# Kernel tuning notes

Hardware: AMD Instinct MI355X
Metric: run time of the kernel (lower is better)

## Reference

```python
import jax, jax.numpy as jnp
import numpy as np

N = 4096
INPLANES = 256
PLANES = 256
LOC_PLANES = 256


def _ln(x, g, b, eps=1e-5):
    m = jnp.mean(x, axis=-1, keepdims=True)
    v = jnp.mean(jnp.square(x - m), axis=-1, keepdims=True)
    return (x - m) * jax.lax.rsqrt(v + eps) * g + b


def setup_inputs() -> dict:
    key = jax.random.key(0)
    ks = jax.random.split(key, 12)
    s = 0.02
    cat_dim = INPLANES + LOC_PLANES
    return {
        "img_fea": jax.random.normal(ks[0], (N, INPLANES), jnp.float32),
        "loc_fea": jax.random.normal(ks[1], (N, LOC_PLANES), jnp.float32),
        # conv11: Basic1d(cat_dim -> inplanes, bias=True) + ReLU
        "w11": jax.random.normal(ks[2], (cat_dim, INPLANES), jnp.float32) * s,
        "b11": jnp.zeros((INPLANES,), jnp.float32),
        # conv12: Linear(inplanes -> inplanes)
        "w12": jax.random.normal(ks[3], (INPLANES, INPLANES), jnp.float32) * s,
        "b12": jnp.zeros((INPLANES,), jnp.float32),
        # conv21: Basic1d(cat_dim -> inplanes, bias=True) + ReLU
        "w21": jax.random.normal(ks[4], (cat_dim, INPLANES), jnp.float32) * s,
        "b21": jnp.zeros((INPLANES,), jnp.float32),
        # conv22: Linear(inplanes -> inplanes*planes) -- hypernetwork weight generator
        "w22": jax.random.normal(ks[5], (INPLANES, INPLANES * PLANES), jnp.float32) * s,
        "b22": jnp.zeros((INPLANES * PLANES,), jnp.float32),
        # br: LayerNorm(planes)
        "lnbr_g": jnp.ones((PLANES,), jnp.float32),
        "lnbr_b": jnp.zeros((PLANES,), jnp.float32),
        # conv3: Basic1d(planes -> planes, bias=False) -> Linear + LayerNorm + ReLU
        "w3": jax.random.normal(ks[6], (PLANES, PLANES), jnp.float32) * s,
        "ln3_g": jnp.ones((PLANES,), jnp.float32),
        "ln3_b": jnp.zeros((PLANES,), jnp.float32),
    }


def reference(img_fea, loc_fea, w11, b11, w12, b12, w21, b21, w22, b22,
              lnbr_g, lnbr_b, w3, ln3_g, ln3_b):
    cat = jnp.concatenate([img_fea, loc_fea], axis=1)          # [N, 512]
    h11 = jax.nn.relu(cat @ w11 + b11)                          # [N, 256]
    wgt12 = h11 @ w12 + b12                                     # [N, 256]
    h21 = jax.nn.relu(cat @ w21 + b21)                          # [N, 256]
    wgt22 = (h21 @ w22 + b22).reshape(-1, INPLANES, PLANES)     # [N, 256, 256]
    out = jnp.einsum('bi,bio->bo', wgt12, wgt22)                # batched GEMV
    out = jax.nn.relu(_ln(out, lnbr_g, lnbr_b))
    out = jax.nn.relu(_ln(out @ w3, ln3_g, ln3_b))
    return (out, loc_fea)
```

## Files before the change

kernel.cpp:

```cpp
#include <hip/hip_runtime.h>
#include <stdint.h>

typedef unsigned short u16;
typedef __bf16 bf16;
typedef bf16 bf16x8 __attribute__((ext_vector_type(8)));
typedef u16 u16x8 __attribute__((ext_vector_type(8)));
typedef float f32x4 __attribute__((ext_vector_type(4)));

__device__ __forceinline__ u16 f2bf(float f) {
  union { float f; unsigned u; } v; v.f = f;
  unsigned u = v.u;
  u += 0x7FFFu + ((u >> 16) & 1u);
  return (u16)(u >> 16);
}

__device__ __forceinline__ bf16x8 as_bf16x8(u16x8 v) {
  return __builtin_bit_cast(bf16x8, v);
}

__device__ __forceinline__ f32x4 mfma16(bf16x8 a, bf16x8 b, f32x4 c) {
  return __builtin_amdgcn_mfma_f32_16x16x32_bf16(a, b, c, 0, 0, 0);
}

__global__ __launch_bounds__(256) void k_transpose(const float* __restrict__ src,
    u16* __restrict__ dst, long dstStride, long dstOff) {
  __shared__ float tile[64][65];
  const int t = threadIdx.x;
  const int tr = t >> 6, tc = t & 63;
  const long rb = (long)blockIdx.x * 64;
  const int ob = blockIdx.y * 64;
#pragma unroll
  for (int i = 0; i < 16; ++i) {
    int r = i * 4 + tr;
    tile[r][tc] = src[(rb + r) * 256 + ob + tc];
  }
  __syncthreads();
  const int orow = t >> 2, seg = t & 3;
#pragma unroll
  for (int h = 0; h < 2; ++h) {
    u16x8 v;
#pragma unroll
    for (int j = 0; j < 8; ++j) v[j] = f2bf(tile[seg * 16 + h * 8 + j][orow]);
    *(u16x8*)&dst[(long)(ob + orow) * dstStride + dstOff + rb + seg * 16 + h * 8] = v;
  }
}

__global__ __launch_bounds__(256) void k_transpose_multi(
    const float* __restrict__ b22, const float* __restrict__ w11,
    const float* __restrict__ w21, const float* __restrict__ w12,
    const float* __restrict__ w3, u16* __restrict__ W2T, u16* __restrict__ W11T,
    u16* __restrict__ W21T, u16* __restrict__ W12T, u16* __restrict__ W3T) {
  __shared__ float tile[64][65];
  const int x = blockIdx.x;
  const float* src; u16* dst; long stride, off; int rb;
  if (x < 4)       { src = b22; dst = W2T;  stride = 65792; off = 65536; rb = x; }
  else if (x < 12) { src = w11; dst = W11T; stride = 512;   off = 0;     rb = x - 4; }
  else if (x < 20) { src = w21; dst = W21T; stride = 512;   off = 0;     rb = x - 12; }
  else if (x < 24) { src = w12; dst = W12T; stride = 256;   off = 0;     rb = x - 20; }
  else             { src = w3;  dst = W3T;  stride = 256;   off = 0;     rb = x - 24; }
  const long rbase = (long)rb * 64;
  const int t = threadIdx.x;
  const int tr = t >> 6, tc = t & 63;
  const int ob = blockIdx.y * 64;
#pragma unroll
  for (int i = 0; i < 16; ++i) {
    int r = i * 4 + tr;
    tile[r][tc] = src[(rbase + r) * 256 + ob + tc];
  }
  __syncthreads();
  const int orow = t >> 2, seg = t & 3;
#pragma unroll
  for (int h = 0; h < 2; ++h) {
    u16x8 v;
#pragma unroll
    for (int j = 0; j < 8; ++j) v[j] = f2bf(tile[seg * 16 + h * 8 + j][orow]);
    *(u16x8*)&dst[(long)(ob + orow) * stride + off + rbase + seg * 16 + h * 8] = v;
  }
}

__device__ __forceinline__ void gemm_small_core(const float* A0, const float* A1,
    int K, const u16* WT, f32x4 (&acc)[4], int o0, long row) {
  const int lane = threadIdx.x & 63;
  const int l15 = lane & 15, lhi = lane >> 4;
  const int kg = lhi * 8;
  for (int ks = 0; ks < K; ks += 32) {
    int k = ks + kg;
    const float* ap = (A1 != nullptr && k >= 256) ? (A1 + row * 256 + (k - 256))
                                                  : (A0 + row * 256 + k);
    f32x4 f0 = *(const f32x4*)ap;
    f32x4 f1 = *(const f32x4*)(ap + 4);
    u16x8 a;
    a[0]=f2bf(f0[0]); a[1]=f2bf(f0[1]); a[2]=f2bf(f0[2]); a[3]=f2bf(f0[3]);
    a[4]=f2bf(f1[0]); a[5]=f2bf(f1[1]); a[6]=f2bf(f1[2]); a[7]=f2bf(f1[3]);
    bf16x8 av = as_bf16x8(a);
#pragma unroll
    for (int nf = 0; nf < 4; ++nf) {
      int o = o0 + nf * 16 + l15;
      u16x8 braw = *(const u16x8*)(WT + (long)o * K + k);
      acc[nf] = mfma16(av, as_bf16x8(braw), acc[nf]);
    }
  }
}

__global__ __launch_bounds__(256) void k_gemm_pair(const float* __restrict__ img,
    const float* __restrict__ loc, const u16* __restrict__ W11T,
    const float* __restrict__ b11, float* __restrict__ h11,
    const u16* __restrict__ W21T, const float* __restrict__ b21,
    float* __restrict__ h21) {
  const int t = threadIdx.x;
  const int wid = t >> 6, lane = t & 63;
  const int l15 = lane & 15, lhi = lane >> 4;
  const int b0 = blockIdx.x * 16;
  const int o0 = wid * 64;
  const long row = b0 + l15;
  const u16* WT = (blockIdx.y == 0) ? W11T : W21T;
  const float* bias = (blockIdx.y == 0) ? b11 : b21;
  float* out = (blockIdx.y == 0) ? h11 : h21;
  f32x4 acc[4] = {};
  gemm_small_core(img, loc, 512, WT, acc, o0, row);
#pragma unroll
  for (int nf = 0; nf < 4; ++nf) {
    int o = o0 + nf * 16 + l15;
    float bs = bias[o];
#pragma unroll
    for (int r = 0; r < 4; ++r) {
      long b = b0 + lhi * 4 + r;
      out[b * 256 + o] = fmaxf(acc[nf][r] + bs, 0.f);
    }
  }
}

__global__ __launch_bounds__(256) void k_gemm_wgt12(const float* __restrict__ h11,
    const u16* __restrict__ W12T, const float* __restrict__ b12,
    u16* __restrict__ wgt12B) {
  const int t = threadIdx.x;
  const int wid = t >> 6, lane = t & 63;
  const int l15 = lane & 15, lhi = lane >> 4;
  const int b0 = blockIdx.x * 16;
  const int o0 = wid * 64;
  const long row = b0 + l15;
  f32x4 acc[4] = {};
  gemm_small_core(h11, nullptr, 256, W12T, acc, o0, row);
#pragma unroll
  for (int nf = 0; nf < 4; ++nf) {
    int o = o0 + nf * 16 + l15;
    float bs = b12[o];
#pragma unroll
    for (int r = 0; r < 4; ++r) {
      long b = b0 + lhi * 4 + r;
      wgt12B[b * 256 + o] = f2bf(acc[nf][r] + bs);
    }
  }
}

__global__ __launch_bounds__(256, 2) void k_big(const u16* __restrict__ W2T,
    const float* __restrict__ h21, const u16* __restrict__ wgt12B,
    float* __restrict__ partials) {
  __shared__ u16 ldsW[128 * 256];
  __shared__ u16 ldsA[128 * 64];
  const int t = threadIdx.x;
  const int wid = t >> 6, lane = t & 63;
  const int l15 = lane & 15, lhi = lane >> 4;
  const int n = blockIdx.x;
  const int chunk = n & 7;
  const int q = n >> 3;
  const int o_base = (q & 1) * 128;
  const int b0 = (q >> 1) * 128;
  const int og = wid >> 1, bg = wid & 1;
  const int nkb = (chunk == 7) ? 33 : 32;
  const int NS = nkb * 4;

  {
    const int r = t >> 1, h = t & 1;
    const u16* src = wgt12B + (long)(b0 + r) * 256 + h * 128;
#pragma unroll
    for (int m = 0; m < 16; ++m) {
      u16x8 v = *(const u16x8*)(src + m * 8);
      const int sg = h * 16 + m;
      const int sw = (sg & 24) | ((sg & 7) ^ (r & 7));
      *(u16x8*)&ldsW[r * 256 + sw * 8] = v;
    }
  }

  const int ar = t >> 1;
  const int ah = t & 1;
  const u16* agbase = W2T + (long)(o_base + ar) * 65792 + chunk * 8192 + ah * 32;
  u16* awbase = ldsA + ar * 64;

  f32x4 acc[4][4] = {};
  u16x8 sa[4];

  auto LOADA = [&](int s) {
    const u16* p = agbase + (long)s * 64;
#pragma unroll
    for (int j = 0; j < 4; ++j) sa[j] = *(const u16x8*)(p + j * 8);
  };
  auto WRITEA = [&]() {
#pragma unroll
    for (int j = 0; j < 4; ++j) {
      const int sg = ah * 4 + j;
      *(u16x8*)&awbase[(sg ^ (ar & 7)) * 8] = sa[j];
    }
  };

  LOADA(0);
  int s = 0;
  for (int kb = 0; kb < nkb; ++kb) {
    const int kk = chunk * 32 + kb;
    float sc[4];
#pragma unroll
    for (int nf = 0; nf < 4; ++nf)
      sc[nf] = (kk < 256)
                 ? h21[(long)(b0 + bg * 64 + nf * 16 + l15) * 256 + kk]
                 : 1.0f;
    f32x4 sub[4][4] = {};
#pragma unroll
    for (int s4 = 0; s4 < 4; ++s4) {
      __syncthreads();
      WRITEA();
      __syncthreads();
      if (s + 1 < NS) LOADA(s + 1);
#pragma unroll
      for (int ksub = 0; ksub < 2; ++ksub) {
        const int x = ksub * 4 + lhi;
        bf16x8 af[4], bv[4];
#pragma unroll
        for (int mf = 0; mf < 4; ++mf) {
          const int ro = og * 64 + mf * 16 + l15;
          af[mf] = as_bf16x8(*(const u16x8*)&ldsA[ro * 64 + ((x ^ (ro & 7)) * 8)]);
        }
#pragma unroll
        for (int nf = 0; nf < 4; ++nf) {
          const int rw = bg * 64 + nf * 16 + l15;
          bv[nf] = as_bf16x8(
              *(const u16x8*)&ldsW[rw * 256 + (s4 * 8 + (x ^ (rw & 7))) * 8]);
        }
        __builtin_amdgcn_s_setprio(1);
#pragma unroll
        for (int mf = 0; mf < 4; ++mf)
#pragma unroll
          for (int nf = 0; nf < 4; ++nf)
            sub[mf][nf] = mfma16(af[mf], bv[nf], sub[mf][nf]);
        __builtin_amdgcn_s_setprio(0);
      }
      ++s;
    }
#pragma unroll
    for (int mf = 0; mf < 4; ++mf)
#pragma unroll
      for (int nf = 0; nf < 4; ++nf)
        acc[mf][nf] += sc[nf] * sub[mf][nf];
  }

  const long cb = (long)chunk * (256L * 4096);
#pragma unroll
  for (int mf = 0; mf < 4; ++mf)
#pragma unroll
    for (int nf = 0; nf < 4; ++nf)
#pragma unroll
      for (int r = 0; r < 4; ++r) {
        const int o = o_base + og * 64 + mf * 16 + lhi * 4 + r;
        const int bgl = b0 + bg * 64 + nf * 16 + l15;
        partials[cb + (long)o * 4096 + bgl] = acc[mf][nf][r];
      }
}

__global__ __launch_bounds__(256) void k_tail(const float* __restrict__ parts,
    const float* __restrict__ lng, const float* __restrict__ lnb,
    const u16* __restrict__ W3T, const float* __restrict__ g3,
    const float* __restrict__ bb3, float* __restrict__ out) {
  __shared__ float tile[16][260];
  __shared__ u16 A16[16][264];
  __shared__ float s1s[4][16], s2s[4][16];
  __shared__ float mz[16], rz[16];
  const int t = threadIdx.x;
  const int b0 = blockIdx.x * 16;
  {
    const int oq = t >> 2, bseg = t & 3;
#pragma unroll
    for (int j = 0; j < 4; ++j) {
      const int o = oq + j * 64;
      f32x4 s = {};
#pragma unroll
      for (int c = 0; c < 8; ++c)
        s += *(const f32x4*)&parts[(long)c * (256L * 4096) + (long)o * 4096 + b0 + bseg * 4];
#pragma unroll
      for (int q = 0; q < 4; ++q) tile[bseg * 4 + q][o] = s[q];
    }
  }
  __syncthreads();
  {
    const int r = t >> 4, og = t & 15;
    float v[16];
    float s1 = 0.f, s2 = 0.f;
#pragma unroll
    for (int q = 0; q < 16; ++q) {
      float x = tile[r][og * 16 + q];
      v[q] = x; s1 += x; s2 += x * x;
    }
    s1 += __shfl_xor(s1, 1); s2 += __shfl_xor(s2, 1);
    s1 += __shfl_xor(s1, 2); s2 += __shfl_xor(s2, 2);
    s1 += __shfl_xor(s1, 4); s2 += __shfl_xor(s2, 4);
    s1 += __shfl_xor(s1, 8); s2 += __shfl_xor(s2, 8);
    float mean = s1 * (1.f / 256.f);
    float var = s2 * (1.f / 256.f) - mean * mean;
    float rstd = rsqrtf(var + 1e-5f);
    u16x8 w0, w1;
#pragma unroll
    for (int q = 0; q < 16; ++q) {
      int o = og * 16 + q;
      float x = (v[q] - mean) * rstd * lng[o] + lnb[o];
      x = fmaxf(x, 0.f);
      if (q < 8) w0[q] = f2bf(x); else w1[q - 8] = f2bf(x);
    }
    *(u16x8*)&A16[r][og * 16] = w0;
    *(u16x8*)&A16[r][og * 16 + 8] = w1;
  }
  __syncthreads();
  const int wid = t >> 6, lane = t & 63;
  const int l15 = lane & 15, lhi = lane >> 4;
  const int wo = wid * 64;
  f32x4 acc[4] = {};
  for (int ks = 0; ks < 256; ks += 32) {
    const int k = ks + lhi * 8;
    bf16x8 av = as_bf16x8(*(const u16x8*)&A16[l15][k]);
#pragma unroll
    for (int nf = 0; nf < 4; ++nf) {
      int o = wo + nf * 16 + l15;
      u16x8 braw = *(const u16x8*)(W3T + (long)o * 256 + k);
      acc[nf] = mfma16(av, as_bf16x8(braw), acc[nf]);
    }
  }
#pragma unroll
  for (int r = 0; r < 4; ++r) {
    float s1 = 0.f, s2 = 0.f;
#pragma unroll
    for (int nf = 0; nf < 4; ++nf) { float x = acc[nf][r]; s1 += x; s2 += x * x; }
    s1 += __shfl_xor(s1, 1); s2 += __shfl_xor(s2, 1);
    s1 += __shfl_xor(s1, 2); s2 += __shfl_xor(s2, 2);
    s1 += __shfl_xor(s1, 4); s2 += __shfl_xor(s2, 4);
    s1 += __shfl_xor(s1, 8); s2 += __shfl_xor(s2, 8);
    if (l15 == 0) { s1s[wid][lhi * 4 + r] = s1; s2s[wid][lhi * 4 + r] = s2; }
  }
  __syncthreads();
  if (t < 16) {
    float s1 = s1s[0][t] + s1s[1][t] + s1s[2][t] + s1s[3][t];
    float s2 = s2s[0][t] + s2s[1][t] + s2s[2][t] + s2s[3][t];
    float mean = s1 * (1.f / 256.f);
    float var = s2 * (1.f / 256.f) - mean * mean;
    mz[t] = mean; rz[t] = rsqrtf(var + 1e-5f);
  }
  __syncthreads();
#pragma unroll
  for (int r = 0; r < 4; ++r) {
    const int b = lhi * 4 + r;
    const float mean = mz[b], rstd = rz[b];
#pragma unroll
    for (int nf = 0; nf < 4; ++nf) {
      int o = wo + nf * 16 + l15;
      float x = (acc[nf][r] - mean) * rstd * g3[o] + bb3[o];
      out[(long)(b0 + b) * 256 + o] = fmaxf(x, 0.f);
    }
  }
}

extern "C" void kernel_launch(void* const* d_in, const int* in_sizes, int n_in,
                              void* d_out, int out_size, void* d_ws, size_t ws_size,
                              hipStream_t stream) {
  const float* img = (const float*)d_in[0];
  const float* loc = (const float*)d_in[1];
  const float* w11 = (const float*)d_in[2];
  const float* b11 = (const float*)d_in[3];
  const float* w12 = (const float*)d_in[4];
  const float* b12 = (const float*)d_in[5];
  const float* w21 = (const float*)d_in[6];
  const float* b21 = (const float*)d_in[7];
  const float* w22 = (const float*)d_in[8];
  const float* b22 = (const float*)d_in[9];
  const float* lng = (const float*)d_in[10];
  const float* lnb = (const float*)d_in[11];
  const float* w3  = (const float*)d_in[12];
  const float* g3  = (const float*)d_in[13];
  const float* bb3 = (const float*)d_in[14];

  char* ws = (char*)d_ws;
  u16* W2T    = (u16*)(ws);
  u16* W11T   = (u16*)(ws + 33685504);
  u16* W21T   = (u16*)(ws + 33947648);
  u16* W12T   = (u16*)(ws + 34209792);
  u16* W3T    = (u16*)(ws + 34340864);
  float* h11  = (float*)(ws + 34471936);
  float* h21  = (float*)(ws + 38666240);
  u16* wgt12B = (u16*)(ws + 42860544);
  float* parts = (float*)(ws + 47054848);
  float* outp  = (float*)d_out;

  hipMemcpyAsync(outp + 1048576, loc, 4194304, hipMemcpyDeviceToDevice, stream);

  hipLaunchKernelGGL(k_transpose, dim3(1024, 4), dim3(256), 0, stream,
                     w22, W2T, (long)65792, (long)0);
  hipLaunchKernelGGL(k_transpose_multi, dim3(28, 4), dim3(256), 0, stream,
                     b22, w11, w21, w12, w3, W2T, W11T, W21T, W12T, W3T);

  hipLaunchKernelGGL(k_gemm_pair, dim3(256, 2), dim3(256), 0, stream,
                     img, loc, W11T, b11, h11, W21T, b21, h21);
  hipLaunchKernelGGL(k_gemm_wgt12, dim3(256), dim3(256), 0, stream,
                     h11, W12T, b12, wgt12B);

  hipLaunchKernelGGL(k_big, dim3(512), dim3(256), 0, stream,
                     W2T, h21, wgt12B, parts);

  hipLaunchKernelGGL(k_tail, dim3(256), dim3(256), 0, stream,
                     parts, lng, lnb, W3T, g3, bb3, outp);
}
```

Measured before the change: 308.7 us.

## Hold wgt12 fragments in registers and double-buffer W2T tiles in LDS

k_big drops the 64 KB LDS copy of wgt12 and keeps each wave's wgt12 B-fragments in registers, split into two halves over the i dimension with an outer loop. The W2T staging tile is now double-buffered in LDS, which cuts the two barriers per step to one. The cost is re-streaming W2T and h21 once per half, plus higher register pressure from the held fragments. It also frees LDS so more blocks can be resident.

```diff
diff --git a/kernel.cpp b/kernel.cpp
--- a/kernel.cpp
+++ b/kernel.cpp
@@ -156,8 +156,7 @@
 __global__ __launch_bounds__(256, 2) void k_big(const u16* __restrict__ W2T,
     const float* __restrict__ h21, const u16* __restrict__ wgt12B,
     float* __restrict__ partials) {
-  __shared__ u16 ldsW[128 * 256];
-  __shared__ u16 ldsA[128 * 64];
+  __shared__ u16 ldsA[2][128 * 64];
   const int t = threadIdx.x;
   const int wid = t >> 6, lane = t & 63;
   const int l15 = lane & 15, lhi = lane >> 4;
@@ -168,88 +167,90 @@
   const int b0 = (q >> 1) * 128;
   const int og = wid >> 1, bg = wid & 1;
   const int nkb = (chunk == 7) ? 33 : 32;
-  const int NS = nkb * 4;
-
-  {
-    const int r = t >> 1, h = t & 1;
-    const u16* src = wgt12B + (long)(b0 + r) * 256 + h * 128;
-#pragma unroll
-    for (int m = 0; m < 16; ++m) {
-      u16x8 v = *(const u16x8*)(src + m * 8);
-      const int sg = h * 16 + m;
-      const int sw = (sg & 24) | ((sg & 7) ^ (r & 7));
-      *(u16x8*)&ldsW[r * 256 + sw * 8] = v;
-    }
-  }
+  const int NS = nkb * 2;
 
   const int ar = t >> 1;
   const int ah = t & 1;
   const u16* agbase = W2T + (long)(o_base + ar) * 65792 + chunk * 8192 + ah * 32;
-  u16* awbase = ldsA + ar * 64;
 
   f32x4 acc[4][4] = {};
   u16x8 sa[4];
 
-  auto LOADA = [&](int s) {
-    const u16* p = agbase + (long)s * 64;
+  auto LOADA = [&](int poff) {
+    const u16* p = agbase + poff;
 #pragma unroll
     for (int j = 0; j < 4; ++j) sa[j] = *(const u16x8*)(p + j * 8);
   };
-  auto WRITEA = [&]() {
+  auto WRITEA = [&](int buf) {
 #pragma unroll
     for (int j = 0; j < 4; ++j) {
       const int sg = ah * 4 + j;
-      *(u16x8*)&awbase[(sg ^ (ar & 7)) * 8] = sa[j];
+      *(u16x8*)&ldsA[buf][ar * 64 + ((sg ^ (ar & 7)) * 8)] = sa[j];
     }
   };
 
-  LOADA(0);
-  int s = 0;
-  for (int kb = 0; kb < nkb; ++kb) {
-    const int kk = chunk * 32 + kb;
-    float sc[4];
-#pragma unroll
-    for (int nf = 0; nf < 4; ++nf)
-      sc[nf] = (kk < 256)
-                 ? h21[(long)(b0 + bg * 64 + nf * 16 + l15) * 256 + kk]
-                 : 1.0f;
-    f32x4 sub[4][4] = {};
-#pragma unroll
-    for (int s4 = 0; s4 < 4; ++s4) {
-      __syncthreads();
-      WRITEA();
-      __syncthreads();
-      if (s + 1 < NS) LOADA(s + 1);
-#pragma unroll
-      for (int ksub = 0; ksub < 2; ++ksub) {
-        const int x = ksub * 4 + lhi;
-        bf16x8 af[4], bv[4];
-#pragma unroll
-        for (int mf = 0; mf < 4; ++mf) {
-          const int ro = og * 64 + mf * 16 + l15;
-          af[mf] = as_bf16x8(*(const u16x8*)&ldsA[ro * 64 + ((x ^ (ro & 7)) * 8)]);
+#pragma unroll 1
+  for (int ih = 0; ih < 2; ++ih) {
+    u16x8 bv[2][2][4];
+#pragma unroll
+    for (int s4 = 0; s4 < 2; ++s4)
+#pragma unroll
+      for (int ksub = 0; ksub < 2; ++ksub)
+#pragma unroll
+        for (int nf = 0; nf < 4; ++nf)
+          bv[s4][ksub][nf] = *(const u16x8*)&wgt12B[
+              (long)(b0 + bg * 64 + nf * 16 + l15) * 256 +
+              ih * 128 + s4 * 64 + ksub * 32 + lhi * 8];
+
+    LOADA(ih * 128);
+    WRITEA(0);
+    __syncthreads();
+
+#pragma unroll 1
+    for (int kb = 0; kb < nkb; ++kb) {
+      const int kk = chunk * 32 + kb;
+      float sc[4];
+#pragma unroll
+      for (int nf = 0; nf < 4; ++nf)
+        sc[nf] = (kk < 256)
+                   ? h21[(long)(b0 + bg * 64 + nf * 16 + l15) * 256 + kk]
+                   : 1.0f;
+      f32x4 sub[4][4] = {};
+#pragma unroll
+      for (int s4 = 0; s4 < 2; ++s4) {
+        const int s = kb * 2 + s4;
+        const int buf = s & 1;
+        if (s + 1 < NS)
+          LOADA((kb * 2 + s4 + 1 >= 2 * (kb + 1) ? (kb + 1) * 256 + ih * 128
+                                                 : kb * 256 + ih * 128 + 64));
+#pragma unroll
+        for (int ksub = 0; ksub < 2; ++ksub) {
+          const int x = ksub * 4 + lhi;
+          bf16x8 af[4];
+#pragma unroll
+          for (int mf = 0; mf < 4; ++mf) {
+            const int ro = og * 64 + mf * 16 + l15;
+            af[mf] = as_bf16x8(
+                *(const u16x8*)&ldsA[buf][ro * 64 + ((x ^ (ro & 7)) * 8)]);
+          }
+          __builtin_amdgcn_s_setprio(1);
+#pragma unroll
+          for (int mf = 0; mf < 4; ++mf)
+#pragma unroll
+            for (int nf = 0; nf < 4; ++nf)
+              sub[mf][nf] = mfma16(af[mf], as_bf16x8(bv[s4][ksub][nf]),
+                                   sub[mf][nf]);
+          __builtin_amdgcn_s_setprio(0);
         }
-#pragma unroll
-        for (int nf = 0; nf < 4; ++nf) {
-          const int rw = bg * 64 + nf * 16 + l15;
-          bv[nf] = as_bf16x8(
-              *(const u16x8*)&ldsW[rw * 256 + (s4 * 8 + (x ^ (rw & 7))) * 8]);
-        }
-        __builtin_amdgcn_s_setprio(1);
-#pragma unroll
-        for (int mf = 0; mf < 4; ++mf)
-#pragma unroll
-          for (int nf = 0; nf < 4; ++nf)
-            sub[mf][nf] = mfma16(af[mf], bv[nf], sub[mf][nf]);
-        __builtin_amdgcn_s_setprio(0);
+        if (s + 1 < NS) WRITEA(buf ^ 1);
+        __syncthreads();
       }
-      ++s;
-    }
-#pragma unroll
-    for (int mf = 0; mf < 4; ++mf)
-#pragma unroll
-      for (int nf = 0; nf < 4; ++nf)
-        acc[mf][nf] += sc[nf] * sub[mf][nf];
+#pragma unroll
+      for (int mf = 0; mf < 4; ++mf)
+#pragma unroll
+        for (int nf = 0; nf < 4; ++nf)
+          acc[mf][nf] += sc[nf] * sub[mf][nf];
+    }
   }
 
   const long cb = (long)chunk * (256L * 4096);
```

Result: slower. 417.7 us (+35.3%).
